# Optimization experiments

Hardware: AMD Instinct MI355X
Metric: run time of the kernel (lower is better)

Reference implementation:

```python
import jax, jax.numpy as jnp
import numpy as np

N_NODES = 100000
N_EDGES = 1600000
D = 128  # node_feat_size == edge_hidden_size


def setup_inputs() -> dict:
    key = jax.random.key(0)
    ks = jax.random.split(key, 10)
    s = 1.0 / np.sqrt(D)
    return {
        "node_feats": jax.random.normal(ks[0], (N_NODES, D), jnp.float32),
        "edge_logits": jax.random.normal(ks[1], (N_EDGES, 1), jnp.float32),
        "W_proj": jax.random.normal(ks[2], (D, D), jnp.float32) * s,
        "b_proj": jax.random.normal(ks[3], (D,), jnp.float32) * s,
        "W1": jax.random.normal(ks[4], (2 * D, D), jnp.float32) * s,
        "b1": jax.random.normal(ks[5], (D,), jnp.float32) * s,
        "W2": jax.random.normal(ks[6], (D, D), jnp.float32) * s,
        "b2": jax.random.normal(ks[7], (D,), jnp.float32) * s,
        "src": jax.random.randint(ks[8], (N_EDGES,), 0, N_NODES),
        "dst": jax.random.randint(ks[9], (N_EDGES,), 0, N_NODES),
    }


def reference(node_feats, edge_logits, W_proj, b_proj, W1, b1, W2, b2, src, dst):
    # ---- edge_softmax: softmax of edge_logits grouped by destination node ----
    # [E,1] logits; per-dst max for numerical stability (gradient-free shift)
    m = jax.ops.segment_max(edge_logits, dst, num_segments=N_NODES)  # [N,1]
    m = jnp.where(jnp.isfinite(m), m, 0.0)  # nodes with no in-edges
    e = jnp.exp(edge_logits - jax.lax.stop_gradient(m)[dst])  # [E,1]
    z = jax.ops.segment_sum(e, dst, num_segments=N_NODES)  # [N,1]
    a = e / z[dst]  # [E,1]

    # ---- project_node (dropout is identity at inference) ----
    hv = node_feats @ W_proj + b_proj  # [N,D]

    # ---- src_mul_edge + sum aggregation: c[v] = sum_{(u->v)} a_uv * hv[u] ----
    msg = hv[src] * a  # [E,D]
    c = jax.ops.segment_sum(msg, dst, num_segments=N_NODES)  # [N,D]

    context = jax.nn.elu(c)
    x = jnp.concatenate([context, node_feats], axis=1)  # [N,2D]
    h = jax.nn.relu(x @ W1 + b1)  # Linear -> Dropout(id) -> ReLU
    out = jax.nn.relu(h @ W2 + b2)  # Linear -> Dropout(id), outer ReLU
    return out
```

## Files before the change

kernel.cpp:

```cpp
#include <hip/hip_runtime.h>
#include <hip/hip_bf16.h>

typedef __hip_bfloat16 bf16;
typedef __attribute__((ext_vector_type(8))) __bf16 bf16x8;
typedef __attribute__((ext_vector_type(4))) float floatx4;

#define BUCKET_SHIFT 7
#define BUCKET_NODES 128
#define MAX_NB 1024

__device__ __forceinline__ unsigned short f2b(float f) {
    bf16 h = __float2bfloat16(f);
    unsigned short s;
    __builtin_memcpy(&s, &h, 2);
    return s;
}
__device__ __forceinline__ float b2f(unsigned short u) {
    unsigned int x = ((unsigned int)u) << 16;
    float f;
    __builtin_memcpy(&f, &x, 4);
    return f;
}
__device__ __forceinline__ float load_dual(const void* p, long long i, bool isbf) {
    return isbf ? b2f(((const unsigned short*)p)[i]) : ((const float*)p)[i];
}
__device__ __forceinline__ bf16x8 ldsfrag(const unsigned short* p) {
    union { uint4 u; bf16x8 v; } t;
    t.u = *(const uint4*)p;
    return t.v;
}
__device__ __forceinline__ bf16x8 gfrag_dual(const void* A, int row, int stride, int k0, bool isbf) {
    if (isbf) {
        union { uint4 u; bf16x8 v; } t;
        t.u = *(const uint4*)((const unsigned short*)A + (size_t)row * stride + k0);
        return t.v;
    }
    const float* ap = (const float*)A + (size_t)row * stride + k0;
    float4 v0 = ((const float4*)ap)[0];
    float4 v1 = ((const float4*)ap)[1];
    union { unsigned short s[8]; bf16x8 v; } t;
    t.s[0] = f2b(v0.x); t.s[1] = f2b(v0.y); t.s[2] = f2b(v0.z); t.s[3] = f2b(v0.w);
    t.s[4] = f2b(v1.x); t.s[5] = f2b(v1.y); t.s[6] = f2b(v1.z); t.s[7] = f2b(v1.w);
    return t.v;
}

__global__ __launch_bounds__(64) void detect_kernel(const unsigned int* __restrict__ words,
                                                    int* __restrict__ flag) {
    int cnt = 0;
    for (int i = threadIdx.x; i < 4096; i += 64) {
        unsigned int lo = words[i] & 0xFFFFu;
        unsigned int e = (lo >> 7) & 0xFFu;
        if (lo == 0u || (e >= 110u && e <= 135u)) cnt++;
    }
#pragma unroll
    for (int off = 32; off > 0; off >>= 1) cnt += __shfl_down(cnt, off, 64);
    if (threadIdx.x == 0) *flag = (cnt > 2458) ? 1 : 0;
}

__global__ __launch_bounds__(256) void transpose_all_kernel(const void* __restrict__ Wp,
                                                            const void* __restrict__ W1,
                                                            const void* __restrict__ W2,
                                                            unsigned short* __restrict__ Wtp,
                                                            unsigned short* __restrict__ Wt1,
                                                            unsigned short* __restrict__ Wt2,
                                                            const int* __restrict__ flag) {
    bool isbf = (*flag != 0);
    int idx = blockIdx.x * 256 + threadIdx.x;
    if (idx < 16384) {
        int n = idx >> 7, k = idx & 127;
        Wtp[idx] = f2b(load_dual(Wp, (long long)k * 128 + n, isbf));
    } else if (idx < 49152) {
        int j = idx - 16384;
        int n = j >> 8, k = j & 255;
        Wt1[j] = f2b(load_dual(W1, (long long)k * 128 + n, isbf));
    } else if (idx < 65536) {
        int j = idx - 49152;
        int n = j >> 7, k = j & 127;
        Wt2[j] = f2b(load_dual(W2, (long long)k * 128 + n, isbf));
    }
}

__global__ __launch_bounds__(256) void bhist_kernel(const int* __restrict__ dst,
                                                    int* __restrict__ bcount, int E) {
    __shared__ int lcnt[MAX_NB];
    for (int i = threadIdx.x; i < MAX_NB; i += 256) lcnt[i] = 0;
    __syncthreads();
    int base = blockIdx.x * 8192;
#pragma unroll
    for (int j = 0; j < 32; ++j) {
        int e = base + j * 256 + threadIdx.x;
        if (e < E) atomicAdd(&lcnt[dst[e] >> BUCKET_SHIFT], 1);
    }
    __syncthreads();
    for (int i = threadIdx.x; i < MAX_NB; i += 256)
        if (lcnt[i]) atomicAdd(&bcount[i], lcnt[i]);
}

__global__ __launch_bounds__(256) void bscan_kernel(const int* __restrict__ bcount,
                                                    int* __restrict__ bstart,
                                                    int* __restrict__ bcursor, int NB) {
    int t = threadIdx.x;
    int v[4];
    int sum = 0;
#pragma unroll
    for (int j = 0; j < 4; ++j) {
        int i = t * 4 + j;
        v[j] = (i < NB) ? bcount[i] : 0;
        sum += v[j];
    }
    int lane = t & 63, wave = t >> 6;
    int inc = sum;
#pragma unroll
    for (int off = 1; off < 64; off <<= 1) {
        int x = __shfl_up(inc, off, 64);
        if (lane >= off) inc += x;
    }
    __shared__ int wsum[4];
    if (lane == 63) wsum[wave] = inc;
    __syncthreads();
    int woff = 0;
    for (int w = 0; w < wave; ++w) woff += wsum[w];
    int run = inc - sum + woff;
#pragma unroll
    for (int j = 0; j < 4; ++j) {
        int i = t * 4 + j;
        if (i < NB) { bstart[i] = run; bcursor[i] = run; }
        run += v[j];
    }
}

__global__ __launch_bounds__(256) void bappend_kernel(const int* __restrict__ dst,
                                                      const int* __restrict__ src,
                                                      const void* __restrict__ logits,
                                                      int* __restrict__ bcursor,
                                                      uint2* __restrict__ ebuf,
                                                      const int* __restrict__ flag, int E) {
    __shared__ int lcnt[MAX_NB];
    __shared__ int lbase[MAX_NB];
    for (int i = threadIdx.x; i < MAX_NB; i += 256) lcnt[i] = 0;
    __syncthreads();
    const bool isbf = (*flag != 0);
    int base = blockIdx.x * 8192;
#pragma unroll
    for (int j = 0; j < 32; ++j) {
        int e = base + j * 256 + threadIdx.x;
        if (e < E) atomicAdd(&lcnt[dst[e] >> BUCKET_SHIFT], 1);
    }
    __syncthreads();
    for (int i = threadIdx.x; i < MAX_NB; i += 256) {
        int c = lcnt[i];
        if (c) { lbase[i] = atomicAdd(&bcursor[i], c); lcnt[i] = 0; }
    }
    __syncthreads();
#pragma unroll
    for (int j = 0; j < 32; ++j) {
        int e = base + j * 256 + threadIdx.x;
        if (e < E) {
            int d = dst[e];
            int b = d >> BUCKET_SHIFT;
            float w = expf(load_dual(logits, e, isbf));
            int pos = lbase[b] + atomicAdd(&lcnt[b], 1);
            uint2 rec;
            rec.x = (unsigned int)src[e] | ((unsigned int)(d & (BUCKET_NODES - 1)) << 24);
            rec.y = __float_as_uint(w);
            ebuf[pos] = rec;
        }
    }
}

__global__ __launch_bounds__(256) void bcsr_kernel(const uint2* __restrict__ ebuf,
                                                   const int* __restrict__ bstart,
                                                   const int* __restrict__ bcount,
                                                   uint2* __restrict__ ebuf2,
                                                   int* __restrict__ row_start,
                                                   int* __restrict__ ncount, int N) {
    __shared__ int lcnt[BUCKET_NODES];
    __shared__ int lbase[BUCKET_NODES];
    const int b = blockIdx.x;
    const int s0 = bstart[b];
    const int cnt = bcount[b];
    if (threadIdx.x < BUCKET_NODES) lcnt[threadIdx.x] = 0;
    __syncthreads();
    for (int i = threadIdx.x; i < cnt; i += 256)
        atomicAdd(&lcnt[ebuf[s0 + i].x >> 24], 1);
    __syncthreads();
    if (threadIdx.x < 64) {
        int lane = threadIdx.x;
        int carry = 0;
#pragma unroll
        for (int half = 0; half < 2; ++half) {
            int idx = half * 64 + lane;
            int v = lcnt[idx];
            int inc = v;
#pragma unroll
            for (int off = 1; off < 64; off <<= 1) {
                int t = __shfl_up(inc, off, 64);
                if (lane >= off) inc += t;
            }
            lbase[idx] = carry + inc - v;
            carry += __shfl(inc, 63, 64);
        }
    }
    __syncthreads();
    if (threadIdx.x < BUCKET_NODES) {
        int gn = b * BUCKET_NODES + threadIdx.x;
        if (gn < N) {
            row_start[gn] = s0 + lbase[threadIdx.x];
            ncount[gn] = lcnt[threadIdx.x];
        }
    }
    __syncthreads();
    if (threadIdx.x < BUCKET_NODES) lcnt[threadIdx.x] = 0;
    __syncthreads();
    for (int i = threadIdx.x; i < cnt; i += 256) {
        uint2 rec = ebuf[s0 + i];
        int dl = rec.x >> 24;
        int pos = lbase[dl] + atomicAdd(&lcnt[dl], 1);
        ebuf2[s0 + pos] = make_uint2(rec.x & 0xFFFFFFu, rec.y);
    }
}

__global__ __launch_bounds__(256) void agg_csr_kernel(const int* __restrict__ row_start,
                                                      const int* __restrict__ ncount,
                                                      const uint2* __restrict__ erec,
                                                      const unsigned int* __restrict__ hv32,
                                                      unsigned int* __restrict__ ctx32, int N) {
    int n = blockIdx.x * 4 + (threadIdx.x >> 6);
    int lane = threadIdx.x & 63;
    if (n >= N) return;
    int s0 = row_start[n];
    int deg = ncount[n];
    float accx = 0.f, accy = 0.f, z = 0.f;
    int i = 0;
    for (; i + 8 <= deg; i += 8) {
        uint2 r[8];
        unsigned int h[8];
#pragma unroll
        for (int j = 0; j < 8; ++j) r[j] = erec[s0 + i + j];
#pragma unroll
        for (int j = 0; j < 8; ++j) h[j] = hv32[(size_t)r[j].x * 64 + lane];
#pragma unroll
        for (int j = 0; j < 8; ++j) {
            float w = __uint_as_float(r[j].y);
            z += w;
            accx += w * b2f((unsigned short)h[j]);
            accy += w * b2f((unsigned short)(h[j] >> 16));
        }
    }
    for (; i + 4 <= deg; i += 4) {
        uint2 r[4];
        unsigned int h[4];
#pragma unroll
        for (int j = 0; j < 4; ++j) r[j] = erec[s0 + i + j];
#pragma unroll
        for (int j = 0; j < 4; ++j) h[j] = hv32[(size_t)r[j].x * 64 + lane];
#pragma unroll
        for (int j = 0; j < 4; ++j) {
            float w = __uint_as_float(r[j].y);
            z += w;
            accx += w * b2f((unsigned short)h[j]);
            accy += w * b2f((unsigned short)(h[j] >> 16));
        }
    }
    for (; i < deg; ++i) {
        uint2 r = erec[s0 + i];
        unsigned int h = hv32[(size_t)r.x * 64 + lane];
        float w = __uint_as_float(r.y);
        z += w;
        accx += w * b2f((unsigned short)h);
        accy += w * b2f((unsigned short)(h >> 16));
    }
    float rz = (z > 0.f) ? 1.f / z : 0.f;
    float x = accx * rz, y = accy * rz;
    x = x > 0.f ? x : expm1f(x);
    y = y > 0.f ? y : expm1f(y);
    ctx32[(size_t)n * 64 + lane] = ((unsigned int)f2b(y) << 16) | f2b(x);
}

__global__ __launch_bounds__(256) void gemm_proj(const void* __restrict__ A,
                                                 const unsigned short* __restrict__ Wt,
                                                 const void* __restrict__ bias,
                                                 unsigned short* __restrict__ hv,
                                                 const int* __restrict__ flag, int N) {
    __shared__ unsigned short Wl[128 * 136];
    const bool isbf = (*flag != 0);
    const int t = threadIdx.x, wid = t >> 6, lane = t & 63;
    const int m16 = lane & 15, quad = lane >> 4;
    const int row0 = blockIdx.x * 128;
    {
        int r = t >> 1, kh = (t & 1) * 64;
        const uint4* s = (const uint4*)(Wt + (size_t)r * 128 + kh);
        uint4* d = (uint4*)&Wl[r * 136 + kh];
#pragma unroll
        for (int q = 0; q < 8; ++q) d[q] = s[q];
    }
    __syncthreads();

    floatx4 acc[2][8];
#pragma unroll
    for (int i = 0; i < 2; ++i)
#pragma unroll
        for (int j = 0; j < 8; ++j) acc[i][j] = (floatx4){0.f, 0.f, 0.f, 0.f};

    int ra0 = row0 + wid * 32 + m16;      if (ra0 >= N) ra0 = N - 1;
    int ra1 = row0 + wid * 32 + 16 + m16; if (ra1 >= N) ra1 = N - 1;

#pragma unroll
    for (int c = 0; c < 4; ++c) {
        int k0 = c * 32 + quad * 8;
        bf16x8 a0 = gfrag_dual(A, ra0, 128, k0, isbf);
        bf16x8 a1 = gfrag_dual(A, ra1, 128, k0, isbf);
#pragma unroll
        for (int nt = 0; nt < 8; ++nt) {
            bf16x8 b = ldsfrag(&Wl[(nt * 16 + m16) * 136 + k0]);
            acc[0][nt] = __builtin_amdgcn_mfma_f32_16x16x32_bf16(a0, b, acc[0][nt], 0, 0, 0);
            acc[1][nt] = __builtin_amdgcn_mfma_f32_16x16x32_bf16(a1, b, acc[1][nt], 0, 0, 0);
        }
    }

#pragma unroll
    for (int mt = 0; mt < 2; ++mt) {
        int gr0 = row0 + wid * 32 + mt * 16 + quad * 4;
#pragma unroll
        for (int nt = 0; nt < 8; ++nt) {
            int col = nt * 16 + m16;
            float bb = load_dual(bias, col, isbf);
#pragma unroll
            for (int rg = 0; rg < 4; ++rg) {
                int gr = gr0 + rg;
                if (gr < N) hv[(size_t)gr * 128 + col] = f2b(acc[mt][nt][rg] + bb);
            }
        }
    }
}

__global__ __launch_bounds__(256) void mlp_fused(const unsigned short* __restrict__ ctx,
                                                 const void* __restrict__ nf,
                                                 const unsigned short* __restrict__ Wt1,
                                                 const void* __restrict__ b1,
                                                 const unsigned short* __restrict__ Wt2,
                                                 const void* __restrict__ b2,
                                                 void* __restrict__ outp,
                                                 const int* __restrict__ flag, int N) {
    __shared__ unsigned short Wl[128 * 72];
    __shared__ unsigned short Hl[4][32 * 136];
    const bool isbf = (*flag != 0);
    const int t = threadIdx.x, wid = t >> 6, lane = t & 63;
    const int m16 = lane & 15, quad = lane >> 4;
    const int row0 = blockIdx.x * 128;

    floatx4 acc[2][8];
#pragma unroll
    for (int i = 0; i < 2; ++i)
#pragma unroll
        for (int j = 0; j < 8; ++j) acc[i][j] = (floatx4){0.f, 0.f, 0.f, 0.f};

    int ra0 = row0 + wid * 32 + m16;      if (ra0 >= N) ra0 = N - 1;
    int ra1 = row0 + wid * 32 + 16 + m16; if (ra1 >= N) ra1 = N - 1;

#pragma unroll
    for (int kc = 0; kc < 4; ++kc) {
        {
            int r = t >> 1, kh = (t & 1) * 32;
            const uint4* s = (const uint4*)(Wt1 + (size_t)r * 256 + kc * 64 + kh);
            uint4* d = (uint4*)&Wl[r * 72 + kh];
#pragma unroll
            for (int q = 0; q < 4; ++q) d[q] = s[q];
        }
        __syncthreads();
#pragma unroll
        for (int c = 0; c < 2; ++c) {
            int kl = c * 32 + quad * 8;
            int ka = kc * 64 + kl;
            bf16x8 a0, a1;
            if (ka < 128) {
                union { uint4 u; bf16x8 v; } t0, t1;
                t0.u = *(const uint4*)(ctx + (size_t)ra0 * 128 + ka);
                t1.u = *(const uint4*)(ctx + (size_t)ra1 * 128 + ka);
                a0 = t0.v; a1 = t1.v;
            } else {
                a0 = gfrag_dual(nf, ra0, 128, ka - 128, isbf);
                a1 = gfrag_dual(nf, ra1, 128, ka - 128, isbf);
            }
#pragma unroll
            for (int nt = 0; nt < 8; ++nt) {
                bf16x8 b = ldsfrag(&Wl[(nt * 16 + m16) * 72 + kl]);
                acc[0][nt] = __builtin_amdgcn_mfma_f32_16x16x32_bf16(a0, b, acc[0][nt], 0, 0, 0);
                acc[1][nt] = __builtin_amdgcn_mfma_f32_16x16x32_bf16(a1, b, acc[1][nt], 0, 0, 0);
            }
        }
        __syncthreads();
    }

#pragma unroll
    for (int nt = 0; nt < 8; ++nt) {
        int col = nt * 16 + m16;
        float bb = load_dual(b1, col, isbf);
#pragma unroll
        for (int mt = 0; mt < 2; ++mt) {
#pragma unroll
            for (int rg = 0; rg < 4; ++rg) {
                int lr = mt * 16 + quad * 4 + rg;
                float x = acc[mt][nt][rg] + bb;
                Hl[wid][lr * 136 + col] = f2b(x > 0.f ? x : 0.f);
            }
        }
    }

#pragma unroll
    for (int i = 0; i < 2; ++i)
#pragma unroll
        for (int j = 0; j < 8; ++j) acc[i][j] = (floatx4){0.f, 0.f, 0.f, 0.f};

#pragma unroll
    for (int kc = 0; kc < 2; ++kc) {
        {
            int r = t >> 1, kh = (t & 1) * 32;
            const uint4* s = (const uint4*)(Wt2 + (size_t)r * 128 + kc * 64 + kh);
            uint4* d = (uint4*)&Wl[r * 72 + kh];
#pragma unroll
            for (int q = 0; q < 4; ++q) d[q] = s[q];
        }
        __syncthreads();
#pragma unroll
        for (int c = 0; c < 2; ++c) {
            int kl = c * 32 + quad * 8;
            int ka = kc * 64 + kl;
            bf16x8 a0 = ldsfrag(&Hl[wid][m16 * 136 + ka]);
            bf16x8 a1 = ldsfrag(&Hl[wid][(16 + m16) * 136 + ka]);
#pragma unroll
            for (int nt = 0; nt < 8; ++nt) {
                bf16x8 b = ldsfrag(&Wl[(nt * 16 + m16) * 72 + kl]);
                acc[0][nt] = __builtin_amdgcn_mfma_f32_16x16x32_bf16(a0, b, acc[0][nt], 0, 0, 0);
                acc[1][nt] = __builtin_amdgcn_mfma_f32_16x16x32_bf16(a1, b, acc[1][nt], 0, 0, 0);
            }
        }
        __syncthreads();
    }

#pragma unroll
    for (int mt = 0; mt < 2; ++mt) {
        int gr0 = row0 + wid * 32 + mt * 16 + quad * 4;
#pragma unroll
        for (int nt = 0; nt < 8; ++nt) {
            int col = nt * 16 + m16;
            float bb = load_dual(b2, col, isbf);
#pragma unroll
            for (int rg = 0; rg < 4; ++rg) {
                int gr = gr0 + rg;
                if (gr < N) {
                    float x = acc[mt][nt][rg] + bb;
                    x = x > 0.f ? x : 0.f;
                    if (!isbf) ((float*)outp)[(size_t)gr * 128 + col] = x;
                    else       ((unsigned short*)outp)[(size_t)gr * 128 + col] = f2b(x);
                }
            }
        }
    }
}

extern "C" void kernel_launch(void* const* d_in, const int* in_sizes, int n_in,
                              void* d_out, int out_size, void* d_ws, size_t ws_size,
                              hipStream_t stream) {
    const void* node_feats  = d_in[0];
    const void* edge_logits = d_in[1];
    const void* W_proj      = d_in[2];
    const void* b_proj      = d_in[3];
    const void* W1          = d_in[4];
    const void* b1          = d_in[5];
    const void* W2          = d_in[6];
    const void* b2          = d_in[7];
    const int*  src         = (const int*)d_in[8];
    const int*  dst         = (const int*)d_in[9];

    const int N = in_sizes[0] / 128;
    const int E = in_sizes[8];
    const int NB = (N + BUCKET_NODES - 1) / BUCKET_NODES;

    char* ws = (char*)d_ws;
    size_t off = 0;
    unsigned short* hv  = (unsigned short*)(ws + off); off += (size_t)N * 256;
    unsigned short* ctx = (unsigned short*)(ws + off); off += (size_t)N * 256;
    uint2* ebuf  = (uint2*)(ws + off); off += (size_t)E * 8;
    uint2* ebuf2 = (uint2*)(ws + off); off += (size_t)E * 8;
    unsigned short* Wtp = (unsigned short*)(ws + off); off += 128 * 128 * 2;
    unsigned short* Wt1 = (unsigned short*)(ws + off); off += 128 * 256 * 2;
    unsigned short* Wt2 = (unsigned short*)(ws + off); off += 128 * 128 * 2;
    int* bcount    = (int*)(ws + off); off += MAX_NB * 4;
    int* bstart    = (int*)(ws + off); off += MAX_NB * 4;
    int* bcursor   = (int*)(ws + off); off += MAX_NB * 4;
    int* row_start = (int*)(ws + off); off += (size_t)N * 4;
    int* ncount    = (int*)(ws + off); off += (size_t)N * 4;
    int* flag      = (int*)(ws + off);

    const int gblocks = (N + 127) / 128;
    const int ebblocks = (E + 8191) / 8192;

    detect_kernel<<<1, 64, 0, stream>>>((const unsigned int*)node_feats, flag);
    hipMemsetAsync(bcount, 0, MAX_NB * 4, stream);

    transpose_all_kernel<<<256, 256, 0, stream>>>(W_proj, W1, W2, Wtp, Wt1, Wt2, flag);

    bhist_kernel<<<ebblocks, 256, 0, stream>>>(dst, bcount, E);
    bscan_kernel<<<1, 256, 0, stream>>>(bcount, bstart, bcursor, NB);
    bappend_kernel<<<ebblocks, 256, 0, stream>>>(dst, src, edge_logits, bcursor,
                                                 ebuf, flag, E);
    bcsr_kernel<<<NB, 256, 0, stream>>>(ebuf, bstart, bcount, ebuf2,
                                        row_start, ncount, N);

    gemm_proj<<<gblocks, 256, 0, stream>>>(node_feats, Wtp, b_proj, hv, flag, N);

    agg_csr_kernel<<<(N + 3) / 4, 256, 0, stream>>>(row_start, ncount, ebuf2,
                                                    (const unsigned int*)hv,
                                                    (unsigned int*)ctx, N);

    mlp_fused<<<gblocks, 256, 0, stream>>>(ctx, node_feats, Wt1, b1, Wt2, b2,
                                           d_out, flag, N);
}
```

Measured before the change: 350.8 us.

## Aggregate raw node features before projection and fuse projection into MLP kernel

Uses linearity to reorder projection and aggregation: the softmax-weighted sum of bf16 node features is computed first, and the W_proj projection plus bias and ELU is applied per node inside the fused MLP kernel. Nodes with no in-edges are masked to zero. A bf16 copy of node features is produced in a kernel merged with the destination histogram, and the bcount memset is folded into detect_kernel. This removes the separate projection GEMM and the hv/ctx round trips, at the cost of an extra cast pass and more work and LDS pressure in the MLP kernel.

```diff
diff --git a/kernel.cpp b/kernel.cpp
--- a/kernel.cpp
+++ b/kernel.cpp
@@ -8,6 +8,7 @@
 #define BUCKET_SHIFT 7
 #define BUCKET_NODES 128
 #define MAX_NB 1024
+#define CAST_BLOCKS 512
 
 __device__ __forceinline__ unsigned short f2b(float f) {
     bf16 h = __float2bfloat16(f);
@@ -45,7 +46,9 @@
 }
 
 __global__ __launch_bounds__(64) void detect_kernel(const unsigned int* __restrict__ words,
-                                                    int* __restrict__ flag) {
+                                                    int* __restrict__ flag,
+                                                    int* __restrict__ bcount) {
+    for (int i = threadIdx.x; i < MAX_NB; i += 64) bcount[i] = 0;
     int cnt = 0;
     for (int i = threadIdx.x; i < 4096; i += 64) {
         unsigned int lo = words[i] & 0xFFFFu;
@@ -80,12 +83,34 @@
     }
 }
 
-__global__ __launch_bounds__(256) void bhist_kernel(const int* __restrict__ dst,
-                                                    int* __restrict__ bcount, int E) {
+__global__ __launch_bounds__(256) void cast_hist_kernel(const void* __restrict__ nf,
+                                                        unsigned short* __restrict__ nfb,
+                                                        const int* __restrict__ dst,
+                                                        int* __restrict__ bcount,
+                                                        const int* __restrict__ flag,
+                                                        int E, int N) {
+    const bool isbf = (*flag != 0);
+    if (blockIdx.x < CAST_BLOCKS) {
+        const int units = N * 16;
+        for (int u = blockIdx.x * 256 + threadIdx.x; u < units; u += CAST_BLOCKS * 256) {
+            if (isbf) {
+                ((uint4*)nfb)[u] = ((const uint4*)nf)[u];
+            } else {
+                const float* ap = (const float*)nf + (size_t)u * 8;
+                float4 v0 = ((const float4*)ap)[0];
+                float4 v1 = ((const float4*)ap)[1];
+                union { uint4 q; unsigned short s[8]; } P;
+                P.s[0] = f2b(v0.x); P.s[1] = f2b(v0.y); P.s[2] = f2b(v0.z); P.s[3] = f2b(v0.w);
+                P.s[4] = f2b(v1.x); P.s[5] = f2b(v1.y); P.s[6] = f2b(v1.z); P.s[7] = f2b(v1.w);
+                ((uint4*)nfb)[u] = P.q;
+            }
+        }
+        return;
+    }
     __shared__ int lcnt[MAX_NB];
     for (int i = threadIdx.x; i < MAX_NB; i += 256) lcnt[i] = 0;
     __syncthreads();
-    int base = blockIdx.x * 8192;
+    int base = (blockIdx.x - CAST_BLOCKS) * 8192;
 #pragma unroll
     for (int j = 0; j < 32; ++j) {
         int e = base + j * 256 + threadIdx.x;
@@ -223,8 +248,8 @@
 __global__ __launch_bounds__(256) void agg_csr_kernel(const int* __restrict__ row_start,
                                                       const int* __restrict__ ncount,
                                                       const uint2* __restrict__ erec,
-                                                      const unsigned int* __restrict__ hv32,
-                                                      unsigned int* __restrict__ ctx32, int N) {
+                                                      const unsigned int* __restrict__ nfb32,
+                                                      unsigned int* __restrict__ g32, int N) {
     int n = blockIdx.x * 4 + (threadIdx.x >> 6);
     int lane = threadIdx.x & 63;
     if (n >= N) return;
@@ -238,7 +263,7 @@
 #pragma unroll
         for (int j = 0; j < 8; ++j) r[j] = erec[s0 + i + j];
 #pragma unroll
-        for (int j = 0; j < 8; ++j) h[j] = hv32[(size_t)r[j].x * 64 + lane];
+        for (int j = 0; j < 8; ++j) h[j] = nfb32[(size_t)r[j].x * 64 + lane];
 #pragma unroll
         for (int j = 0; j < 8; ++j) {
             float w = __uint_as_float(r[j].y);
@@ -253,7 +278,7 @@
 #pragma unroll
         for (int j = 0; j < 4; ++j) r[j] = erec[s0 + i + j];
 #pragma unroll
-        for (int j = 0; j < 4; ++j) h[j] = hv32[(size_t)r[j].x * 64 + lane];
+        for (int j = 0; j < 4; ++j) h[j] = nfb32[(size_t)r[j].x * 64 + lane];
 #pragma unroll
         for (int j = 0; j < 4; ++j) {
             float w = __uint_as_float(r[j].y);
@@ -264,84 +289,28 @@
     }
     for (; i < deg; ++i) {
         uint2 r = erec[s0 + i];
-        unsigned int h = hv32[(size_t)r.x * 64 + lane];
+        unsigned int h = nfb32[(size_t)r.x * 64 + lane];
         float w = __uint_as_float(r.y);
         z += w;
         accx += w * b2f((unsigned short)h);
         accy += w * b2f((unsigned short)(h >> 16));
     }
     float rz = (z > 0.f) ? 1.f / z : 0.f;
-    float x = accx * rz, y = accy * rz;
-    x = x > 0.f ? x : expm1f(x);
-    y = y > 0.f ? y : expm1f(y);
-    ctx32[(size_t)n * 64 + lane] = ((unsigned int)f2b(y) << 16) | f2b(x);
-}
-
-__global__ __launch_bounds__(256) void gemm_proj(const void* __restrict__ A,
-                                                 const unsigned short* __restrict__ Wt,
-                                                 const void* __restrict__ bias,
-                                                 unsigned short* __restrict__ hv,
-                                                 const int* __restrict__ flag, int N) {
-    __shared__ unsigned short Wl[128 * 136];
-    const bool isbf = (*flag != 0);
-    const int t = threadIdx.x, wid = t >> 6, lane = t & 63;
-    const int m16 = lane & 15, quad = lane >> 4;
-    const int row0 = blockIdx.x * 128;
-    {
-        int r = t >> 1, kh = (t & 1) * 64;
-        const uint4* s = (const uint4*)(Wt + (size_t)r * 128 + kh);
-        uint4* d = (uint4*)&Wl[r * 136 + kh];
-#pragma unroll
-        for (int q = 0; q < 8; ++q) d[q] = s[q];
-    }
-    __syncthreads();
-
-    floatx4 acc[2][8];
-#pragma unroll
-    for (int i = 0; i < 2; ++i)
-#pragma unroll
-        for (int j = 0; j < 8; ++j) acc[i][j] = (floatx4){0.f, 0.f, 0.f, 0.f};
-
-    int ra0 = row0 + wid * 32 + m16;      if (ra0 >= N) ra0 = N - 1;
-    int ra1 = row0 + wid * 32 + 16 + m16; if (ra1 >= N) ra1 = N - 1;
-
-#pragma unroll
-    for (int c = 0; c < 4; ++c) {
-        int k0 = c * 32 + quad * 8;
-        bf16x8 a0 = gfrag_dual(A, ra0, 128, k0, isbf);
-        bf16x8 a1 = gfrag_dual(A, ra1, 128, k0, isbf);
-#pragma unroll
-        for (int nt = 0; nt < 8; ++nt) {
-            bf16x8 b = ldsfrag(&Wl[(nt * 16 + m16) * 136 + k0]);
-            acc[0][nt] = __builtin_amdgcn_mfma_f32_16x16x32_bf16(a0, b, acc[0][nt], 0, 0, 0);
-            acc[1][nt] = __builtin_amdgcn_mfma_f32_16x16x32_bf16(a1, b, acc[1][nt], 0, 0, 0);
-        }
-    }
-
-#pragma unroll
-    for (int mt = 0; mt < 2; ++mt) {
-        int gr0 = row0 + wid * 32 + mt * 16 + quad * 4;
-#pragma unroll
-        for (int nt = 0; nt < 8; ++nt) {
-            int col = nt * 16 + m16;
-            float bb = load_dual(bias, col, isbf);
-#pragma unroll
-            for (int rg = 0; rg < 4; ++rg) {
-                int gr = gr0 + rg;
-                if (gr < N) hv[(size_t)gr * 128 + col] = f2b(acc[mt][nt][rg] + bb);
-            }
-        }
-    }
-}
-
-__global__ __launch_bounds__(256) void mlp_fused(const unsigned short* __restrict__ ctx,
-                                                 const void* __restrict__ nf,
-                                                 const unsigned short* __restrict__ Wt1,
-                                                 const void* __restrict__ b1,
-                                                 const unsigned short* __restrict__ Wt2,
-                                                 const void* __restrict__ b2,
-                                                 void* __restrict__ outp,
-                                                 const int* __restrict__ flag, int N) {
+    g32[(size_t)n * 64 + lane] =
+        ((unsigned int)f2b(accy * rz) << 16) | f2b(accx * rz);
+}
+
+__global__ __launch_bounds__(256) void mega_mlp(const unsigned short* __restrict__ g,
+                                                const void* __restrict__ nf,
+                                                const int* __restrict__ ncount,
+                                                const unsigned short* __restrict__ Wtp,
+                                                const void* __restrict__ bp,
+                                                const unsigned short* __restrict__ Wt1,
+                                                const void* __restrict__ b1,
+                                                const unsigned short* __restrict__ Wt2,
+                                                const void* __restrict__ b2,
+                                                void* __restrict__ outp,
+                                                const int* __restrict__ flag, int N) {
     __shared__ unsigned short Wl[128 * 72];
     __shared__ unsigned short Hl[4][32 * 136];
     const bool isbf = (*flag != 0);
@@ -359,6 +328,59 @@
     int ra1 = row0 + wid * 32 + 16 + m16; if (ra1 >= N) ra1 = N - 1;
 
 #pragma unroll
+    for (int kc = 0; kc < 2; ++kc) {
+        {
+            int r = t >> 1, kh = (t & 1) * 32;
+            const uint4* s = (const uint4*)(Wtp + (size_t)r * 128 + kc * 64 + kh);
+            uint4* d = (uint4*)&Wl[r * 72 + kh];
+#pragma unroll
+            for (int q = 0; q < 4; ++q) d[q] = s[q];
+        }
+        __syncthreads();
+#pragma unroll
+        for (int c = 0; c < 2; ++c) {
+            int kl = c * 32 + quad * 8;
+            int ka = kc * 64 + kl;
+            union { uint4 u; bf16x8 v; } t0, t1;
+            t0.u = *(const uint4*)(g + (size_t)ra0 * 128 + ka);
+            t1.u = *(const uint4*)(g + (size_t)ra1 * 128 + ka);
+#pragma unroll
+            for (int nt = 0; nt < 8; ++nt) {
+                bf16x8 b = ldsfrag(&Wl[(nt * 16 + m16) * 72 + kl]);
+                acc[0][nt] = __builtin_amdgcn_mfma_f32_16x16x32_bf16(t0.v, b, acc[0][nt], 0, 0, 0);
+                acc[1][nt] = __builtin_amdgcn_mfma_f32_16x16x32_bf16(t1.v, b, acc[1][nt], 0, 0, 0);
+            }
+        }
+        __syncthreads();
+    }
+
+#pragma unroll
+    for (int mt = 0; mt < 2; ++mt) {
+#pragma unroll
+        for (int rg = 0; rg < 4; ++rg) {
+            int lr = mt * 16 + quad * 4 + rg;
+            int gr = row0 + wid * 32 + lr;
+            if (gr >= N) gr = N - 1;
+            int deg = ncount[gr];
+#pragma unroll
+            for (int nt = 0; nt < 8; ++nt) {
+                int col = nt * 16 + m16;
+                float x = 0.f;
+                if (deg > 0) {
+                    x = acc[mt][nt][rg] + load_dual(bp, col, isbf);
+                    x = x > 0.f ? x : expm1f(x);
+                }
+                Hl[wid][lr * 136 + col] = f2b(x);
+            }
+        }
+    }
+
+#pragma unroll
+    for (int i = 0; i < 2; ++i)
+#pragma unroll
+        for (int j = 0; j < 8; ++j) acc[i][j] = (floatx4){0.f, 0.f, 0.f, 0.f};
+
+#pragma unroll
     for (int kc = 0; kc < 4; ++kc) {
         {
             int r = t >> 1, kh = (t & 1) * 32;
@@ -374,10 +396,8 @@
             int ka = kc * 64 + kl;
             bf16x8 a0, a1;
             if (ka < 128) {
-                union { uint4 u; bf16x8 v; } t0, t1;
-                t0.u = *(const uint4*)(ctx + (size_t)ra0 * 128 + ka);
-                t1.u = *(const uint4*)(ctx + (size_t)ra1 * 128 + ka);
-                a0 = t0.v; a1 = t1.v;
+                a0 = ldsfrag(&Hl[wid][m16 * 136 + ka]);
+                a1 = ldsfrag(&Hl[wid][(16 + m16) * 136 + ka]);
             } else {
                 a0 = gfrag_dual(nf, ra0, 128, ka - 128, isbf);
                 a1 = gfrag_dual(nf, ra1, 128, ka - 128, isbf);
@@ -479,8 +499,8 @@
 
     char* ws = (char*)d_ws;
     size_t off = 0;
-    unsigned short* hv  = (unsigned short*)(ws + off); off += (size_t)N * 256;
-    unsigned short* ctx = (unsigned short*)(ws + off); off += (size_t)N * 256;
+    unsigned short* nfb = (unsigned short*)(ws + off); off += (size_t)N * 256;
+    unsigned short* g   = (unsigned short*)(ws + off); off += (size_t)N * 256;
     uint2* ebuf  = (uint2*)(ws + off); off += (size_t)E * 8;
     uint2* ebuf2 = (uint2*)(ws + off); off += (size_t)E * 8;
     unsigned short* Wtp = (unsigned short*)(ws + off); off += 128 * 128 * 2;
@@ -496,24 +516,21 @@
     const int gblocks = (N + 127) / 128;
     const int ebblocks = (E + 8191) / 8192;
 
-    detect_kernel<<<1, 64, 0, stream>>>((const unsigned int*)node_feats, flag);
-    hipMemsetAsync(bcount, 0, MAX_NB * 4, stream);
-
+    detect_kernel<<<1, 64, 0, stream>>>((const unsigned int*)node_feats, flag, bcount);
     transpose_all_kernel<<<256, 256, 0, stream>>>(W_proj, W1, W2, Wtp, Wt1, Wt2, flag);
 
-    bhist_kernel<<<ebblocks, 256, 0, stream>>>(dst, bcount, E);
+    cast_hist_kernel<<<CAST_BLOCKS + ebblocks, 256, 0, stream>>>(
+        node_feats, nfb, dst, bcount, flag, E, N);
     bscan_kernel<<<1, 256, 0, stream>>>(bcount, bstart, bcursor, NB);
     bappend_kernel<<<ebblocks, 256, 0, stream>>>(dst, src, edge_logits, bcursor,
                                                  ebuf, flag, E);
     bcsr_kernel<<<NB, 256, 0, stream>>>(ebuf, bstart, bcount, ebuf2,
                                         row_start, ncount, N);
 
-    gemm_proj<<<gblocks, 256, 0, stream>>>(node_feats, Wtp, b_proj, hv, flag, N);
-
     agg_csr_kernel<<<(N + 3) / 4, 256, 0, stream>>>(row_start, ncount, ebuf2,
-                                                    (const unsigned int*)hv,
-                                                    (unsigned int*)ctx, N);
-
-    mlp_fused<<<gblocks, 256, 0, stream>>>(ctx, node_feats, Wt1, b1, Wt2, b2,
-                                           d_out, flag, N);
-}
+                                                    (const unsigned int*)nfb,
+                                                    (unsigned int*)g, N);
+
+    mega_mlp<<<gblocks, 256, 0, stream>>>(g, node_feats, ncount, Wtp, b_proj,
+                                          Wt1, b1, Wt2, b2, d_out, flag, N);
+}
```

After: 354.7 us. No clear change (+1.1%).
